# Kernel optimization log

Measured on AMD Instinct MI355X. Metric: run time of the kernel, lower is better.

Reference implementation:

```python
import jax, jax.numpy as jnp
import numpy as np

TP, TN = 0.03, 0.03   # top-k fractions (module init args)
TS, TC = 0.03, 0.07   # sigmoid sharpness, contrastive temperature
EPS_PD = 1e-6         # torch F.pairwise_distance eps


def _l2norm(x, axis):
    # F.normalize(p=2) with eps clamp 1e-12
    return x / jnp.maximum(jnp.linalg.norm(x, axis=axis, keepdims=True), 1e-12)


def setup_inputs() -> dict:
    key = jax.random.key(0)
    k = jax.random.split(key, 5)
    B, C, H, W = 192, 512, 28, 28
    return {
        "ev": jax.random.normal(k[0], (B, C, H, W), jnp.float32),
        "ea": jax.random.normal(k[1], (B, 2048), jnp.float32),
        "Wv": jax.random.normal(k[2], (C, C), jnp.float32) * 0.04,
        "Wa1": jax.random.normal(k[3], (512, 2048), jnp.float32) * 0.02,
        "Wa2": jax.random.normal(k[4], (512, 512), jnp.float32) * 0.04,
    }


def reference(ev, ea, Wv, Wa1, Wa2):
    B, C, H, W = ev.shape
    HW = H * W
    tp = int(HW * TP)
    tn = int(HW * TN)

    # audio projection (frozen encoder output ea -> fa)
    fa = jax.nn.relu(ea @ Wa1.T) @ Wa2.T            # [B, 512]

    # visual 1x1-conv projection + GAP
    fv_map = jnp.einsum('bchw,oc->bohw', ev, Wv)    # [B, C, H, W]
    ind_vec = fv_map.mean(axis=(2, 3))              # [B, C]

    fv_norm = _l2norm(fv_map, axis=1)               # per-pixel channel L2 norm
    iv_norm = _l2norm(ind_vec, axis=1)              # [B, C]

    # Sij[b,d,p] = <fv_norm[b,:,p], iv_norm[d,:]>
    S = jnp.einsum('bchw,dc->bdhw', fv_norm, iv_norm).reshape(B, B, HW)

    # data-dependent per-(b,d) top-k thresholds
    pos_thr = jax.lax.top_k(S, tp)[0][..., -1:]     # tp-th largest
    neg_thr = -jax.lax.top_k(-S, tn)[0][..., -1:]   # tn-th smallest

    m_p = jax.nn.sigmoid((S - pos_thr) / TS)
    m_n = 1.0 - jax.nn.sigmoid((S - neg_thr) / TS)

    SP = (S * m_p).sum(-1) / m_p.sum(-1)            # [B, B]
    SN = (S * m_n).sum(-1) / m_n.sum(-1)            # [B, B]

    logits1 = jnp.concatenate([SP, SN], axis=1) / TC      # [B, 2B]
    logits2 = jnp.concatenate([SP.T, SN.T], axis=1) / TC  # [B, 2B]
    labels = jnp.arange(B)

    def ce(logits):
        logp = jax.nn.log_softmax(logits, axis=-1)
        return -jnp.take_along_axis(logp, labels[:, None], axis=1).mean()

    loss1 = ce(logits1)
    loss2 = ce(logits2)

    eye = jnp.eye(B, dtype=S.dtype)
    mask = eye - (1.0 - eye) / (B - 1)

    # squared pairwise distance between detached ind_vec and fa (torch eps)
    iv_d = jax.lax.stop_gradient(ind_vec)
    diff = iv_d[:, None, :] - fa[None, :, :] + EPS_PD
    dist = (diff * diff).sum(-1)                    # [B, B]

    ivn_d = jax.lax.stop_gradient(iv_norm)
    vv = ivn_d @ ivn_d.T
    w = -vv * (1.0 - eye) + eye
    dist = dist * w

    loss3 = jnp.maximum((dist * mask).sum(1) + 0.6, 0.0).mean()
    loss4 = jnp.maximum((dist * mask).sum(0) + 0.6, 0.0).mean()

    return ((loss1 + loss2) / 2, (loss3 + loss4) / 2)
```

## Files before the change

kernel.cpp:

```cpp
#include <hip/hip_runtime.h>
#include <hip/hip_fp8.h>
#include <math.h>

#define B_   192
#define C_   512
#define HW_  784
#define TPK  23
#define NTOT (B_ * HW_)

typedef __attribute__((ext_vector_type(4))) float f4;
typedef __attribute__((ext_vector_type(8))) unsigned char uc8;

__device__ __forceinline__ float sigf(float x) {
    return 1.0f / (1.0f + __expf(-x));
}
__device__ __forceinline__ unsigned short f2bf(float f) {
    unsigned u = __float_as_uint(f);
    unsigned r = u + 0x7FFFu + ((u >> 16) & 1u);
    return (unsigned short)(r >> 16);
}
__device__ __forceinline__ float bf2f(unsigned short u) {
    return __uint_as_float(((unsigned)u) << 16);
}
__device__ __forceinline__ unsigned char f2fp8(float x) {
    __hip_fp8_e4m3 t(x);
    return (unsigned char)t.__x;
}
__device__ __forceinline__ void gld16(const void* g, void* l) {
    __builtin_amdgcn_global_load_lds((const __attribute__((address_space(1))) unsigned int*)g,
                                     (__attribute__((address_space(3))) unsigned int*)l, 16, 0, 0);
}

__global__ void k_evmean(const float* __restrict__ ev, float* __restrict__ evmean) {
    int row  = blockIdx.x * 4 + (threadIdx.x >> 6);
    int lane = threadIdx.x & 63;
    const float4* s4 = (const float4*)(ev + (size_t)row * HW_);
    float s = 0.f;
    for (int i = lane; i < HW_ / 4; i += 64) {
        float4 v = s4[i];
        s += v.x + v.y + v.z + v.w;
    }
    for (int off = 32; off > 0; off >>= 1) s += __shfl_down(s, off, 64);
    if (lane == 0) evmean[row] = s * (1.0f / HW_);
}

template<int BKN, int RELUA, int SPLITK>
__global__ __launch_bounds__(256)
void k32(const float* __restrict__ A, const float* __restrict__ B,
         float* __restrict__ C, int M, int N, int K) {
    __shared__ float As[16][68];
    __shared__ float Bs[16][68];
    int m0 = blockIdx.y * 64, n0 = blockIdx.x * 64;
    int kslice = K / SPLITK;
    int kbeg = blockIdx.z * kslice;
    int tid = threadIdx.x;
    int tx = tid & 15, ty = tid >> 4;
    int r = tid >> 2, c4 = tid & 3;

    float acc[4][4];
#pragma unroll
    for (int i = 0; i < 4; i++)
#pragma unroll
        for (int j = 0; j < 4; j++) acc[i][j] = 0.f;

    for (int k0 = kbeg; k0 < kbeg + kslice; k0 += 16) {
        float4 av = *(const float4*)(A + (size_t)(m0 + r) * K + k0 + c4 * 4);
        if (RELUA) {
            av.x = fmaxf(av.x, 0.f); av.y = fmaxf(av.y, 0.f);
            av.z = fmaxf(av.z, 0.f); av.w = fmaxf(av.w, 0.f);
        }
        As[c4 * 4 + 0][r] = av.x; As[c4 * 4 + 1][r] = av.y;
        As[c4 * 4 + 2][r] = av.z; As[c4 * 4 + 3][r] = av.w;
        if (BKN == 0) {
            float4 bv = *(const float4*)(B + (size_t)(n0 + r) * K + k0 + c4 * 4);
            Bs[c4 * 4 + 0][r] = bv.x; Bs[c4 * 4 + 1][r] = bv.y;
            Bs[c4 * 4 + 2][r] = bv.z; Bs[c4 * 4 + 3][r] = bv.w;
        } else {
            float4 bv = *(const float4*)(B + (size_t)(k0 + ty) * N + n0 + tx * 4);
            Bs[ty][tx * 4 + 0] = bv.x; Bs[ty][tx * 4 + 1] = bv.y;
            Bs[ty][tx * 4 + 2] = bv.z; Bs[ty][tx * 4 + 3] = bv.w;
        }
        __syncthreads();
#pragma unroll
        for (int kk = 0; kk < 16; kk++) {
            float a_[4];
#pragma unroll
            for (int i = 0; i < 4; i++) a_[i] = As[kk][ty * 4 + i];
            float4 bb = *(const float4*)&Bs[kk][tx * 4];
#pragma unroll
            for (int i = 0; i < 4; i++) {
                acc[i][0] = fmaf(a_[i], bb.x, acc[i][0]);
                acc[i][1] = fmaf(a_[i], bb.y, acc[i][1]);
                acc[i][2] = fmaf(a_[i], bb.z, acc[i][2]);
                acc[i][3] = fmaf(a_[i], bb.w, acc[i][3]);
            }
        }
        __syncthreads();
    }
#pragma unroll
    for (int i = 0; i < 4; i++) {
        if (SPLITK > 1) {
            float* row = C + (size_t)(m0 + ty * 4 + i) * N + n0 + tx * 4;
#pragma unroll
            for (int j = 0; j < 4; j++) atomicAdd(&row[j], acc[i][j]);
        } else {
            *(float4*)(C + (size_t)(m0 + ty * 4 + i) * N + n0 + tx * 4) =
                make_float4(acc[i][0], acc[i][1], acc[i][2], acc[i][3]);
        }
    }
}

__global__ void k_rownorm(const float* __restrict__ iv, float* __restrict__ ivn) {
    int b = blockIdx.x, lane = threadIdx.x;
    float v[8]; float s = 0.f;
#pragma unroll
    for (int k = 0; k < 8; k++) {
        v[k] = iv[(size_t)b * C_ + lane + 64 * k];
        s = fmaf(v[k], v[k], s);
    }
#pragma unroll
    for (int off = 32; off > 0; off >>= 1) s += __shfl_xor(s, off, 64);
    float rn = 1.0f / fmaxf(sqrtf(s), 1e-12f);
#pragma unroll
    for (int k = 0; k < 8; k++) ivn[(size_t)b * C_ + lane + 64 * k] = v[k] * rn;
}

__global__ void k_prepA(const float* __restrict__ Wv, unsigned char* __restrict__ Abf) {
    int r = blockIdx.x, tid = threadIdx.x;
    int row = (r < 512) ? r : (192 + r);
    for (int i = 0; i < 2; i++) {
        int c = tid + i * 256;
        float v = (r < 512) ? Wv[(size_t)r * C_ + c] : 0.f;
        Abf[(size_t)row * C_ + c] = f2fp8(v);
    }
}

__global__ __launch_bounds__(256)
void k_Ufp8(const float* __restrict__ ivn, const float* __restrict__ Wv,
            unsigned char* __restrict__ Abf) {
    __shared__ float As[16][68];
    __shared__ float Bs[16][68];
    int m0 = blockIdx.y * 64, n0 = blockIdx.x * 64;
    int tid = threadIdx.x;
    int tx = tid & 15, ty = tid >> 4;
    int r = tid >> 2, c4 = tid & 3;
    float acc[4][4];
#pragma unroll
    for (int i = 0; i < 4; i++)
#pragma unroll
        for (int j = 0; j < 4; j++) acc[i][j] = 0.f;
    for (int k0 = 0; k0 < C_; k0 += 16) {
        float4 av = *(const float4*)(ivn + (size_t)(m0 + r) * C_ + k0 + c4 * 4);
        As[c4 * 4 + 0][r] = av.x; As[c4 * 4 + 1][r] = av.y;
        As[c4 * 4 + 2][r] = av.z; As[c4 * 4 + 3][r] = av.w;
        float4 bv = *(const float4*)(Wv + (size_t)(k0 + ty) * C_ + n0 + tx * 4);
        Bs[ty][tx * 4 + 0] = bv.x; Bs[ty][tx * 4 + 1] = bv.y;
        Bs[ty][tx * 4 + 2] = bv.z; Bs[ty][tx * 4 + 3] = bv.w;
        __syncthreads();
#pragma unroll
        for (int kk = 0; kk < 16; kk++) {
            float a_[4];
#pragma unroll
            for (int i = 0; i < 4; i++) a_[i] = As[kk][ty * 4 + i];
            float4 bb = *(const float4*)&Bs[kk][tx * 4];
#pragma unroll
            for (int i = 0; i < 4; i++) {
                acc[i][0] = fmaf(a_[i], bb.x, acc[i][0]);
                acc[i][1] = fmaf(a_[i], bb.y, acc[i][1]);
                acc[i][2] = fmaf(a_[i], bb.z, acc[i][2]);
                acc[i][3] = fmaf(a_[i], bb.w, acc[i][3]);
            }
        }
        __syncthreads();
    }
#pragma unroll
    for (int i = 0; i < 4; i++) {
        unsigned char* row = Abf + (size_t)(512 + m0 + ty * 4 + i) * C_ + n0 + tx * 4;
#pragma unroll
        for (int j = 0; j < 4; j++) row[j] = f2fp8(acc[i][j]);
    }
}

__global__ __launch_bounds__(256)
void k_transpose64(const float* __restrict__ ev, unsigned char* __restrict__ evT,
                   float* __restrict__ evsum, int doevm, int b0) {
    __shared__ float t[64][67];
    int bl = blockIdx.z, b = b0 + bl;
    int c0 = blockIdx.y * 64, p0 = blockIdx.x * 64;
    int tid = threadIdx.x;
    int cl = tid >> 4;
    int pc = tid & 15;
    int p = p0 + pc * 4;
#pragma unroll
    for (int q = 0; q < 4; q++) {
        int c_local = q * 16 + cl;
        const float* src = ev + ((size_t)b * C_ + c0 + c_local) * HW_;
        float4 v = make_float4(0.f, 0.f, 0.f, 0.f);
        if (p + 3 < HW_) v = *(const float4*)(src + p);
        else if (p < HW_) { for (int j = 0; j < 4; j++) if (p + j < HW_) ((float*)&v)[j] = src[p + j]; }
        if (doevm) {
            float rs = v.x + v.y + v.z + v.w;
            rs += __shfl_xor(rs, 1, 16);
            rs += __shfl_xor(rs, 2, 16);
            rs += __shfl_xor(rs, 4, 16);
            rs += __shfl_xor(rs, 8, 16);
            if (pc == 0) atomicAdd(&evsum[b * C_ + c0 + c_local], rs * (1.0f / HW_));
        }
        t[c_local][pc * 4 + 0] = v.x; t[c_local][pc * 4 + 1] = v.y;
        t[c_local][pc * 4 + 2] = v.z; t[c_local][pc * 4 + 3] = v.w;
    }
    __syncthreads();
    int r = tid >> 3;
    int j = tid & 7;
#pragma unroll
    for (int q = 0; q < 2; q++) {
        int prow = p0 + r + q * 32;
        if (prow < HW_) {
            uc8 o;
#pragma unroll
            for (int k = 0; k < 8; k++) o[k] = f2fp8(t[j * 8 + k][r + q * 32]);
            *(uc8*)(evT + ((size_t)bl * HW_ + prow) * C_ + c0 + j * 8) = o;
        }
    }
}

__global__ __launch_bounds__(256, 4)
void k_gemm(const unsigned char* __restrict__ Abf, const unsigned char* __restrict__ evT,
            float* __restrict__ n2, unsigned short* __restrict__ Tb, int ntiles) {
    __shared__ unsigned char As[2][4096];
    __shared__ unsigned char Bs[2][4096];

    int id = blockIdx.x;
    int xcd = id & 7, slot = id >> 3;
    int S = (ntiles + 7) >> 3;
    int w = xcd * S + slot;
    if (w >= ntiles) return;
    int nt = w / 6, ot = w % 6;
    int o0 = ot * 128, n0 = nt * 128;

    int tid = threadIdx.x;
    int wid = tid >> 6, lane = tid & 63;
    int wy = wid >> 1, wx = wid & 1;
    int l15 = lane & 15, l4 = lane >> 4;

    const unsigned char* Ag = Abf + ((size_t)o0 + (tid >> 1)) * C_ + (tid & 1) * 16;
    const unsigned char* Bg = evT + ((size_t)n0 + (tid >> 1)) * C_ + (tid & 1) * 16;
    int lds_off = tid * 16;

    f4 acc[4][4] = {};
    int cur = 0;

#define STAGE(buf, k0) do { \
    gld16(Ag + (k0), &As[buf][0] + lds_off); \
    gld16(Bg + (k0), &Bs[buf][0] + lds_off); \
} while (0)

    STAGE(0, 0);
    __syncthreads();
    for (int t = 0; t < 16; ++t) {
        if (t < 15) STAGE(cur ^ 1, (t + 1) * 32);
        const long* Ar = (const long*)&As[cur][0];
        const long* Br = (const long*)&Bs[cur][0];
        long a[4], b[4];
#pragma unroll
        for (int mi = 0; mi < 4; mi++) a[mi] = Ar[(wy * 64 + mi * 16 + l15) * 4 + l4];
#pragma unroll
        for (int ni = 0; ni < 4; ni++) b[ni] = Br[(wx * 64 + ni * 16 + l15) * 4 + l4];
#pragma unroll
        for (int mi = 0; mi < 4; mi++)
#pragma unroll
            for (int ni = 0; ni < 4; ni++)
                acc[mi][ni] = __builtin_amdgcn_mfma_f32_16x16x32_fp8_fp8(a[mi], b[ni], acc[mi][ni], 0, 0, 0);
        __syncthreads();
        cur ^= 1;
    }
#undef STAGE

    if (ot < 4) {
        float* red = (float*)&As[0][0];
#pragma unroll
        for (int ni = 0; ni < 4; ni++) {
            float s = 0.f;
#pragma unroll
            for (int mi = 0; mi < 4; mi++)
#pragma unroll
                for (int r = 0; r < 4; r++) { float x = acc[mi][ni][r]; s = fmaf(x, x, s); }
            red[(wy * 4 + l4) * 128 + wx * 64 + ni * 16 + l15] = s;
        }
        __syncthreads();
        if (tid < 128) {
            float s = 0.f;
#pragma unroll
            for (int q = 0; q < 8; q++) s += red[q * 128 + tid];
            atomicAdd(&n2[n0 + tid], s);
        }
    } else {
        int dbase = o0 - 512 + wy * 64;
        unsigned blv[4]; int pv[4];
#pragma unroll
        for (int ni = 0; ni < 4; ni++) {
            unsigned nn = (unsigned)(n0 + wx * 64 + ni * 16 + l15);
            blv[ni] = nn / 784u;
            pv[ni]  = (int)(nn - blv[ni] * 784u);
        }
#pragma unroll
        for (int mi = 0; mi < 4; mi++)
#pragma unroll
            for (int r = 0; r < 4; r++) {
                int dd = dbase + mi * 16 + l4 * 4 + r;
                if (dd < B_) {
#pragma unroll
                    for (int ni = 0; ni < 4; ni++)
                        Tb[((size_t)blv[ni] * B_ + dd) * HW_ + pv[ni]] = f2bf(acc[mi][ni][r]);
                }
            }
    }
}

__global__ void k_invn(const float* __restrict__ n2, float* __restrict__ invn, int n) {
    int i = blockIdx.x * 256 + threadIdx.x;
    if (i >= n) return;
    invn[i] = 1.0f / fmaxf(sqrtf(n2[i]), 1e-12f);
}

__global__ __launch_bounds__(256)
void k_pool(const unsigned short* __restrict__ T, const float* __restrict__ invn,
            float* __restrict__ SP, float* __restrict__ SN, int b0) {
    int tid = threadIdx.x;
    int wv = tid >> 6, lane = tid & 63;
    int d = blockIdx.x * 4 + wv;
    int bl = blockIdx.y, b = b0 + bl;
    const unsigned short* Trow = T + ((size_t)b * B_ + d) * HW_;
    const float* nrow = invn + (size_t)b * HW_;
    float sv[13];
#pragma unroll
    for (int i = 0; i < 12; i++) {
        int p = lane + i * 64;
        sv[i] = bf2f(Trow[p]) * nrow[p];
    }
    {
        int p = lane + 768;
        sv[12] = (p < HW_) ? bf2f(Trow[p]) * nrow[p] : __uint_as_float(0x7FC00000u);
    }
    float vmax = -1e30f, vmin = 1e30f;
#pragma unroll
    for (int i = 0; i < 13; i++) { vmax = fmaxf(vmax, sv[i]); vmin = fminf(vmin, sv[i]); }
#pragma unroll
    for (int off = 32; off > 0; off >>= 1) {
        vmax = fmaxf(vmax, __shfl_xor(vmax, off, 64));
        vmin = fminf(vmin, __shfl_xor(vmin, off, 64));
    }
    float lo1 = vmin, hi1 = vmax, lo2 = vmin, hi2 = vmax;
    for (int it = 0; it < 13; ++it) {
        float m1 = 0.5f * (lo1 + hi1), m2 = 0.5f * (lo2 + hi2);
        int c1 = 0, c2 = 0;
#pragma unroll
        for (int i = 0; i < 13; i++) {
            c1 += __popcll(__ballot(sv[i] >= m1));
            c2 += __popcll(__ballot(sv[i] <= m2));
        }
        if (c1 >= TPK) lo1 = m1; else hi1 = m1;
        if (c2 >= TPK) hi2 = m2; else lo2 = m2;
    }
    float thrp = lo1, thrn = hi2;
    const float its = 1.0f / 0.03f;
    float spn = 0.f, spd = 0.f, snn = 0.f, snd = 0.f;
#pragma unroll
    for (int i = 0; i < 13; i++) {
        if (i == 12 && lane >= 16) continue;
        float s = sv[i];
        float mp = sigf((s - thrp) * its);
        float mn = sigf(-(s - thrn) * its);
        spn += s * mp; spd += mp;
        snn += s * mn; snd += mn;
    }
    for (int off = 32; off > 0; off >>= 1) {
        spn += __shfl_down(spn, off, 64);
        spd += __shfl_down(spd, off, 64);
        snn += __shfl_down(snn, off, 64);
        snd += __shfl_down(snd, off, 64);
    }
    if (lane == 0) {
        SP[b * B_ + d] = spn / spd;
        SN[b * B_ + d] = snn / snd;
    }
}

__global__ void k_loss12(const float* __restrict__ SP, const float* __restrict__ SN,
                         float* __restrict__ acc) {
    __shared__ float red[128];
    int i = blockIdx.x, tid = threadIdx.x;
    const float itc = 1.0f / 0.07f;
    for (int phase = 0; phase < 2; phase++) {
        float mx = -INFINITY;
        for (int j = tid; j < 2 * B_; j += 128) {
            float v;
            if (phase == 0) v = (j < B_ ? SP[i * B_ + j] : SN[i * B_ + (j - B_)]);
            else            v = (j < B_ ? SP[j * B_ + i] : SN[(j - B_) * B_ + i]);
            mx = fmaxf(mx, v * itc);
        }
        red[tid] = mx; __syncthreads();
        for (int s = 64; s > 0; s >>= 1) { if (tid < s) red[tid] = fmaxf(red[tid], red[tid + s]); __syncthreads(); }
        mx = red[0]; __syncthreads();
        float se = 0.f;
        for (int j = tid; j < 2 * B_; j += 128) {
            float v;
            if (phase == 0) v = (j < B_ ? SP[i * B_ + j] : SN[i * B_ + (j - B_)]);
            else            v = (j < B_ ? SP[j * B_ + i] : SN[(j - B_) * B_ + i]);
            se += __expf(v * itc - mx);
        }
        red[tid] = se; __syncthreads();
        for (int s = 64; s > 0; s >>= 1) { if (tid < s) red[tid] += red[tid + s]; __syncthreads(); }
        if (tid == 0) {
            float lse = logf(red[0]) + mx;
            atomicAdd(&acc[phase], lse - SP[i * B_ + i] * itc);
        }
        __syncthreads();
    }
}

__global__ __launch_bounds__(256)
void k_distfin(const float* __restrict__ iv, const float* __restrict__ ivn,
               const float* __restrict__ fa, const float* __restrict__ acc,
               float* __restrict__ rowsum, float* __restrict__ colsum,
               int* __restrict__ cnt, float* __restrict__ out) {
    __shared__ float Ai[16][68], An[16][68], Bf[16][68], Bn[16][68];
    __shared__ float rred[64][17], cred[64][17];
    __shared__ float fr[256];
    __shared__ int lastf;
    int i0 = blockIdx.y * 64, j0 = blockIdx.x * 64;
    int tid = threadIdx.x;
    int tx = tid & 15, ty = tid >> 4;
    int r = tid >> 2, c4 = tid & 3;
    float accD[4][4], accV[4][4];
#pragma unroll
    for (int i = 0; i < 4; i++)
#pragma unroll
        for (int j = 0; j < 4; j++) { accD[i][j] = 0.f; accV[i][j] = 0.f; }

    for (int k0 = 0; k0 < C_; k0 += 16) {
        float4 v;
        v = *(const float4*)(iv + (size_t)(i0 + r) * C_ + k0 + c4 * 4);
        Ai[c4*4+0][r]=v.x; Ai[c4*4+1][r]=v.y; Ai[c4*4+2][r]=v.z; Ai[c4*4+3][r]=v.w;
        v = *(const float4*)(ivn + (size_t)(i0 + r) * C_ + k0 + c4 * 4);
        An[c4*4+0][r]=v.x; An[c4*4+1][r]=v.y; An[c4*4+2][r]=v.z; An[c4*4+3][r]=v.w;
        v = *(const float4*)(fa + (size_t)(j0 + r) * C_ + k0 + c4 * 4);
        Bf[c4*4+0][r]=v.x; Bf[c4*4+1][r]=v.y; Bf[c4*4+2][r]=v.z; Bf[c4*4+3][r]=v.w;
        v = *(const float4*)(ivn + (size_t)(j0 + r) * C_ + k0 + c4 * 4);
        Bn[c4*4+0][r]=v.x; Bn[c4*4+1][r]=v.y; Bn[c4*4+2][r]=v.z; Bn[c4*4+3][r]=v.w;
        __syncthreads();
#pragma unroll
        for (int kk = 0; kk < 16; kk++) {
            float ai[4], an[4];
#pragma unroll
            for (int i = 0; i < 4; i++) { ai[i] = Ai[kk][ty*4+i]; an[i] = An[kk][ty*4+i]; }
            float4 bf = *(const float4*)&Bf[kk][tx*4];
            float4 bn = *(const float4*)&Bn[kk][tx*4];
#pragma unroll
            for (int i = 0; i < 4; i++) {
                float d0 = ai[i] - bf.x + 1e-6f; accD[i][0] = fmaf(d0, d0, accD[i][0]);
                float d1 = ai[i] - bf.y + 1e-6f; accD[i][1] = fmaf(d1, d1, accD[i][1]);
                float d2 = ai[i] - bf.z + 1e-6f; accD[i][2] = fmaf(d2, d2, accD[i][2]);
                float d3 = ai[i] - bf.w + 1e-6f; accD[i][3] = fmaf(d3, d3, accD[i][3]);
                accV[i][0] = fmaf(an[i], bn.x, accV[i][0]);
                accV[i][1] = fmaf(an[i], bn.y, accV[i][1]);
                accV[i][2] = fmaf(an[i], bn.z, accV[i][2]);
                accV[i][3] = fmaf(an[i], bn.w, accV[i][3]);
            }
        }
        __syncthreads();
    }
    float rp[4] = {0.f, 0.f, 0.f, 0.f};
    float cp[4] = {0.f, 0.f, 0.f, 0.f};
#pragma unroll
    for (int i = 0; i < 4; i++)
#pragma unroll
        for (int j = 0; j < 4; j++) {
            int gi = i0 + ty * 4 + i, gj = j0 + tx * 4 + j;
            float val = (gi == gj) ? accD[i][j] : accD[i][j] * accV[i][j] * (1.0f / 191.0f);
            rp[i] += val; cp[j] += val;
        }
#pragma unroll
    for (int i = 0; i < 4; i++) rred[ty * 4 + i][tx] = rp[i];
#pragma unroll
    for (int j = 0; j < 4; j++) cred[tx * 4 + j][ty] = cp[j];
    __syncthreads();
    if (tid < 64) {
        float s = 0.f;
#pragma unroll
        for (int q = 0; q < 16; q++) s += rred[tid][q];
        atomicAdd(&rowsum[i0 + tid], s);
    } else if (tid < 128) {
        int t = tid - 64;
        float s = 0.f;
#pragma unroll
        for (int q = 0; q < 16; q++) s += cred[t][q];
        atomicAdd(&colsum[j0 + t], s);
    }
    __threadfence();
    __syncthreads();
    if (tid == 0) lastf = (atomicAdd(cnt, 1) == 8);
    __syncthreads();
    if (lastf) {
        __threadfence();
        float v3 = (tid < B_) ? fmaxf(rowsum[tid] + 0.6f, 0.f) : 0.f;
        float v4 = (tid < B_) ? fmaxf(colsum[tid] + 0.6f, 0.f) : 0.f;
        fr[tid] = v3; __syncthreads();
        for (int s = 128; s > 0; s >>= 1) { if (tid < s) fr[tid] += fr[tid + s]; __syncthreads(); }
        float l3 = fr[0] / B_;
        __syncthreads();
        fr[tid] = v4; __syncthreads();
        for (int s = 128; s > 0; s >>= 1) { if (tid < s) fr[tid] += fr[tid + s]; __syncthreads(); }
        float l4 = fr[0] / B_;
        if (tid == 0) {
            out[0] = 0.5f * (acc[0] + acc[1]) / B_;
            out[1] = 0.5f * (l3 + l4);
        }
    }
}

extern "C" void kernel_launch(void* const* d_in, const int* in_sizes, int n_in,
                              void* d_out, int out_size, void* d_ws, size_t ws_size,
                              hipStream_t stream) {
    const float* ev  = (const float*)d_in[0];
    const float* ea  = (const float*)d_in[1];
    const float* Wv  = (const float*)d_in[2];
    const float* Wa1 = (const float*)d_in[3];
    const float* Wa2 = (const float*)d_in[4];
    float* out = (float*)d_out;
    float* ws  = (float*)d_ws;

    size_t off = 0;
    float* evmean  = ws + off; off += B_ * C_;
    float* ind_vec = ws + off; off += B_ * C_;
    float* Hb      = ws + off; off += B_ * C_;
    float* fa      = ws + off; off += B_ * C_;
    float* n2      = ws + off; off += NTOT;
    float* accb    = ws + off;
    float* rowsum  = accb + 16;
    float* colsum  = rowsum + B_;
    int*   cntp    = (int*)(colsum + B_);
    off += 16 + B_ + B_ + 16;
    size_t zero_count = off;
    float* iv_norm = ws + off; off += B_ * C_;
    float* invn    = ws + off; off += NTOT;
    float* SPb     = ws + off; off += B_ * B_;
    float* SNb     = ws + off; off += B_ * B_;
    unsigned char* Abf = (unsigned char*)(ws + off); off += 768 * C_ / 4;

    size_t perB_f = (size_t)HW_ * C_ / 4 + (size_t)B_ * HW_ / 2;
    size_t avail  = ws_size / 4 > off ? ws_size / 4 - off : 0;
    int chunk = (int)(avail / perB_f);
    chunk &= ~7;
    if (chunk > B_) chunk = B_;
    if (chunk < 8) chunk = 8;
    unsigned char* evT = (unsigned char*)(ws + off);
    unsigned short* Tb = (unsigned short*)(evT + (size_t)chunk * HW_ * C_);

    hipMemsetAsync(ws, 0, zero_count * sizeof(float), stream);

    k_prepA<<<576, 256, 0, stream>>>(Wv, Abf);

    if (chunk >= B_) {
        dim3 gt(13, C_ / 64, B_);
        k_transpose64<<<gt, 256, 0, stream>>>(ev, evT, evmean, 1, 0);
    } else {
        k_evmean<<<B_ * C_ / 4, 256, 0, stream>>>(ev, evmean);
    }

    k32<0, 0, 4><<<dim3(8, 3, 4), 256, 0, stream>>>(ea, Wa1, Hb, B_, C_, 2048);
    k32<0, 1, 2><<<dim3(8, 3, 2), 256, 0, stream>>>(Hb, Wa2, fa, B_, C_, C_);

    k32<0, 0, 2><<<dim3(8, 3, 2), 256, 0, stream>>>(evmean, Wv, ind_vec, B_, C_, C_);
    k_rownorm<<<B_, 64, 0, stream>>>(ind_vec, iv_norm);
    k_Ufp8<<<dim3(8, 3), 256, 0, stream>>>(iv_norm, Wv, Abf);

    if (chunk >= B_) {
        int ntiles = (NTOT / 128) * 6;
        int S = (ntiles + 7) >> 3;
        k_gemm<<<8 * S, 256, 0, stream>>>(Abf, evT, n2, Tb, ntiles);
        k_invn<<<(NTOT + 255) / 256, 256, 0, stream>>>(n2, invn, NTOT);
        dim3 gp(B_ / 4, B_);
        k_pool<<<gp, 256, 0, stream>>>(Tb, invn, SPb, SNb, 0);
    } else {
        for (int b0 = 0; b0 < B_; b0 += chunk) {
            int nb = (B_ - b0 < chunk) ? (B_ - b0) : chunk;
            dim3 gt(13, C_ / 64, nb);
            k_transpose64<<<gt, 256, 0, stream>>>(ev, evT, evmean, 0, b0);
            int ntiles = (nb * HW_ / 128) * 6;
            int S = (ntiles + 7) >> 3;
            k_gemm<<<8 * S, 256, 0, stream>>>(Abf, evT, n2 + (size_t)b0 * HW_, Tb, ntiles);
            int n = nb * HW_;
            k_invn<<<(n + 255) / 256, 256, 0, stream>>>(n2 + (size_t)b0 * HW_,
                                                        invn + (size_t)b0 * HW_, n);
            dim3 gp(B_ / 4, nb);
            k_pool<<<gp, 256, 0, stream>>>(Tb - (size_t)b0 * B_ * HW_, invn, SPb, SNb, b0);
        }
    }

    k_loss12<<<B_, 128, 0, stream>>>(SPb, SNb, accb);
    dim3 gd(B_ / 64, B_ / 64);
    k_distfin<<<gd, 256, 0, stream>>>(ind_vec, iv_norm, fa, accb, rowsum, colsum, cntp, out);
}
```

Before: 484.4 us.

## Switch fp8 GEMM to 32x32x64 scaled MFMA with swizzled K-64 tiles

Result: faster. 443.9 us (-8.4%).

```diff
diff --git a/kernel.cpp b/kernel.cpp
--- a/kernel.cpp
+++ b/kernel.cpp
@@ -7,8 +7,12 @@
 #define HW_  784
 #define TPK  23
 #define NTOT (B_ * HW_)
+#define SCL  0x7F7F7F7F
 
 typedef __attribute__((ext_vector_type(4))) float f4;
+typedef __attribute__((ext_vector_type(16))) float f16v;
+typedef __attribute__((ext_vector_type(8))) int i8i;
+typedef __attribute__((ext_vector_type(4))) unsigned int u4i;
 typedef __attribute__((ext_vector_type(8))) unsigned char uc8;
 
 __device__ __forceinline__ float sigf(float x) {
@@ -29,6 +33,14 @@
 __device__ __forceinline__ void gld16(const void* g, void* l) {
     __builtin_amdgcn_global_load_lds((const __attribute__((address_space(1))) unsigned int*)g,
                                      (__attribute__((address_space(3))) unsigned int*)l, 16, 0, 0);
+}
+__device__ __forceinline__ i8i frag32(const unsigned char* base, int c0, int c1) {
+    u4i lo = *(const u4i*)(base + c0);
+    u4i hi = *(const u4i*)(base + c1);
+    i8i r;
+    r[0] = (int)lo[0]; r[1] = (int)lo[1]; r[2] = (int)lo[2]; r[3] = (int)lo[3];
+    r[4] = (int)hi[0]; r[5] = (int)hi[1]; r[6] = (int)hi[2]; r[7] = (int)hi[3];
+    return r;
 }
 
 __global__ void k_evmean(const float* __restrict__ ev, float* __restrict__ evmean) {
@@ -128,10 +140,11 @@
 __global__ void k_prepA(const float* __restrict__ Wv, unsigned char* __restrict__ Abf) {
     int r = blockIdx.x, tid = threadIdx.x;
     int row = (r < 512) ? r : (192 + r);
+    int swz = ((row >> 1) & 3) << 4;
     for (int i = 0; i < 2; i++) {
         int c = tid + i * 256;
         float v = (r < 512) ? Wv[(size_t)r * C_ + c] : 0.f;
-        Abf[(size_t)row * C_ + c] = f2fp8(v);
+        Abf[(size_t)row * C_ + (c ^ swz)] = f2fp8(v);
     }
 }
 
@@ -175,9 +188,12 @@
     }
 #pragma unroll
     for (int i = 0; i < 4; i++) {
-        unsigned char* row = Abf + (size_t)(512 + m0 + ty * 4 + i) * C_ + n0 + tx * 4;
-#pragma unroll
-        for (int j = 0; j < 4; j++) row[j] = f2fp8(acc[i][j]);
+        int orow = 512 + m0 + ty * 4 + i;
+        int swz = ((orow >> 1) & 3) << 4;
+        unsigned char* rowp = Abf + (size_t)orow * C_;
+        int cphys = (n0 + tx * 4) ^ swz;
+#pragma unroll
+        for (int j = 0; j < 4; j++) rowp[cphys + j] = f2fp8(acc[i][j]);
     }
 }
 
@@ -216,10 +232,12 @@
     for (int q = 0; q < 2; q++) {
         int prow = p0 + r + q * 32;
         if (prow < HW_) {
+            size_t n = (size_t)bl * HW_ + prow;
+            int swz = ((int)(n >> 1) & 3) << 4;
             uc8 o;
 #pragma unroll
             for (int k = 0; k < 8; k++) o[k] = f2fp8(t[j * 8 + k][r + q * 32]);
-            *(uc8*)(evT + ((size_t)bl * HW_ + prow) * C_ + c0 + j * 8) = o;
+            *(uc8*)(evT + n * C_ + c0 + ((j * 8) ^ swz)) = o;
         }
     }
 }
@@ -227,8 +245,8 @@
 __global__ __launch_bounds__(256, 4)
 void k_gemm(const unsigned char* __restrict__ Abf, const unsigned char* __restrict__ evT,
             float* __restrict__ n2, unsigned short* __restrict__ Tb, int ntiles) {
-    __shared__ unsigned char As[2][4096];
-    __shared__ unsigned char Bs[2][4096];
+    __shared__ unsigned char As[2][8192];
+    __shared__ unsigned char Bs[2][8192];
 
     int id = blockIdx.x;
     int xcd = id & 7, slot = id >> 3;
@@ -241,36 +259,44 @@
     int tid = threadIdx.x;
     int wid = tid >> 6, lane = tid & 63;
     int wy = wid >> 1, wx = wid & 1;
-    int l15 = lane & 15, l4 = lane >> 4;
-
-    const unsigned char* Ag = Abf + ((size_t)o0 + (tid >> 1)) * C_ + (tid & 1) * 16;
-    const unsigned char* Bg = evT + ((size_t)n0 + (tid >> 1)) * C_ + (tid & 1) * 16;
-    int lds_off = tid * 16;
-
-    f4 acc[4][4] = {};
+    int r31 = lane & 31, hi = lane >> 5;
+    int swz = (r31 >> 1) & 3;
+    int ch0 = ((2 * hi) ^ swz) * 16;
+    int ch1 = ((2 * hi + 1) ^ swz) * 16;
+
+    const unsigned char* Ag = Abf + ((size_t)o0 + (tid >> 2)) * C_ + (tid & 3) * 16;
+    const unsigned char* Bg = evT + ((size_t)n0 + (tid >> 2)) * C_ + (tid & 3) * 16;
+    int lds16 = tid * 16;
+
+    f16v acc[2][2] = {};
     int cur = 0;
 
 #define STAGE(buf, k0) do { \
-    gld16(Ag + (k0), &As[buf][0] + lds_off); \
-    gld16(Bg + (k0), &Bs[buf][0] + lds_off); \
+    gld16(Ag + (k0),           &As[buf][0]    + lds16); \
+    gld16(Ag + (k0) + 64 * C_, &As[buf][4096] + lds16); \
+    gld16(Bg + (k0),           &Bs[buf][0]    + lds16); \
+    gld16(Bg + (k0) + 64 * C_, &Bs[buf][4096] + lds16); \
 } while (0)
 
     STAGE(0, 0);
     __syncthreads();
-    for (int t = 0; t < 16; ++t) {
-        if (t < 15) STAGE(cur ^ 1, (t + 1) * 32);
-        const long* Ar = (const long*)&As[cur][0];
-        const long* Br = (const long*)&Bs[cur][0];
-        long a[4], b[4];
-#pragma unroll
-        for (int mi = 0; mi < 4; mi++) a[mi] = Ar[(wy * 64 + mi * 16 + l15) * 4 + l4];
-#pragma unroll
-        for (int ni = 0; ni < 4; ni++) b[ni] = Br[(wx * 64 + ni * 16 + l15) * 4 + l4];
-#pragma unroll
-        for (int mi = 0; mi < 4; mi++)
-#pragma unroll
-            for (int ni = 0; ni < 4; ni++)
-                acc[mi][ni] = __builtin_amdgcn_mfma_f32_16x16x32_fp8_fp8(a[mi], b[ni], acc[mi][ni], 0, 0, 0);
+    for (int t = 0; t < 8; ++t) {
+        if (t < 7) STAGE(cur ^ 1, (t + 1) * 64);
+        const unsigned char* Ab = &As[cur][0];
+        const unsigned char* Bb = &Bs[cur][0];
+        i8i a[2], b[2];
+#pragma unroll
+        for (int mi = 0; mi < 2; mi++)
+            a[mi] = frag32(Ab + (wy * 64 + mi * 32 + r31) * 64, ch0, ch1);
+#pragma unroll
+        for (int ni = 0; ni < 2; ni++)
+            b[ni] = frag32(Bb + (wx * 64 + ni * 32 + r31) * 64, ch0, ch1);
+#pragma unroll
+        for (int mi = 0; mi < 2; mi++)
+#pragma unroll
+            for (int ni = 0; ni < 2; ni++)
+                acc[mi][ni] = __builtin_amdgcn_mfma_scale_f32_32x32x64_f8f6f4(
+                    a[mi], b[ni], acc[mi][ni], 0, 0, 0, SCL, 0, SCL);
         __syncthreads();
         cur ^= 1;
     }
@@ -279,38 +305,38 @@
     if (ot < 4) {
         float* red = (float*)&As[0][0];
 #pragma unroll
-        for (int ni = 0; ni < 4; ni++) {
+        for (int ni = 0; ni < 2; ni++) {
             float s = 0.f;
 #pragma unroll
-            for (int mi = 0; mi < 4; mi++)
-#pragma unroll
-                for (int r = 0; r < 4; r++) { float x = acc[mi][ni][r]; s = fmaf(x, x, s); }
-            red[(wy * 4 + l4) * 128 + wx * 64 + ni * 16 + l15] = s;
+            for (int mi = 0; mi < 2; mi++)
+#pragma unroll
+                for (int r = 0; r < 16; r++) { float x = acc[mi][ni][r]; s = fmaf(x, x, s); }
+            red[(wy * 2 + hi) * 128 + wx * 64 + ni * 32 + r31] = s;
         }
         __syncthreads();
         if (tid < 128) {
             float s = 0.f;
 #pragma unroll
-            for (int q = 0; q < 8; q++) s += red[q * 128 + tid];
+            for (int q = 0; q < 4; q++) s += red[q * 128 + tid];
             atomicAdd(&n2[n0 + tid], s);
         }
     } else {
         int dbase = o0 - 512 + wy * 64;
-        unsigned blv[4]; int pv[4];
-#pragma unroll
-        for (int ni = 0; ni < 4; ni++) {
-            unsigned nn = (unsigned)(n0 + wx * 64 + ni * 16 + l15);
+        unsigned blv[2]; int pv[2];
+#pragma unroll
+        for (int ni = 0; ni < 2; ni++) {
+            unsigned nn = (unsigned)(n0 + wx * 64 + ni * 32 + r31);
             blv[ni] = nn / 784u;
             pv[ni]  = (int)(nn - blv[ni] * 784u);
         }
 #pragma unroll
-        for (int mi = 0; mi < 4; mi++)
-#pragma unroll
-            for (int r = 0; r < 4; r++) {
-                int dd = dbase + mi * 16 + l4 * 4 + r;
+        for (int mi = 0; mi < 2; mi++)
+#pragma unroll
+            for (int r = 0; r < 16; r++) {
+                int dd = dbase + mi * 32 + (r & 3) + 8 * (r >> 2) + 4 * hi;
                 if (dd < B_) {
 #pragma unroll
-                    for (int ni = 0; ni < 4; ni++)
+                    for (int ni = 0; ni < 2; ni++)
                         Tb[((size_t)blv[ni] * B_ + dd) * HW_ + pv[ni]] = f2bf(acc[mi][ni][r]);
                 }
             }
```
